# Kernel optimization log

Measured on AMD Instinct MI355X. Metric: run time of the kernel, lower is better.

## Reference

```python
import jax, jax.numpy as jnp
import numpy as np

DIM = 2048
NUM_HEADS = 16
HEAD_DIM = DIM // NUM_HEADS
WINDOW_SIZE = 3072
SCALE = HEAD_DIM ** (-0.5)
NEG_INF = -1e9


def setup_inputs() -> dict:
    key = jax.random.key(0)
    ks = jax.random.split(key, 6)
    B, N = 2, 2048
    x = jax.random.normal(ks[0], (B, N, DIM), dtype=jnp.float32)
    w_init = 0.02
    Wq = jax.random.normal(ks[1], (DIM, DIM), dtype=jnp.float32) * w_init
    Wk = jax.random.normal(ks[2], (DIM, DIM), dtype=jnp.float32) * w_init
    Wv = jax.random.normal(ks[3], (DIM, DIM), dtype=jnp.float32) * w_init
    Wo = jax.random.normal(ks[4], (DIM, DIM), dtype=jnp.float32) * w_init
    zeros = jnp.zeros((DIM,), dtype=jnp.float32)
    return {"x": x, "Wq": Wq, "bq": zeros, "Wk": Wk, "bk": zeros,
            "Wv": Wv, "bv": zeros, "Wo": Wo, "bo": zeros}


def _window_mask(q_len: int, kv_len: int) -> jnp.ndarray:
    # Faithful to SlidingWindowAttention._window_mask with causal=True:
    # row i allows j in [max(0, kv_len - window_size + i), i]; mask=True means blocked.
    i = jnp.arange(q_len)[:, None]
    j = jnp.arange(kv_len)[None, :]
    start = jnp.maximum(0, kv_len - WINDOW_SIZE + i)
    allowed = (j >= start) & (j <= i)  # second term is the causal triu complement
    return ~allowed  # [q_len, kv_len] bool, True = masked


def reference(x, Wq, bq, Wk, bk, Wv, bv, Wo, bo):
    B, N, C = x.shape
    H, D = NUM_HEADS, HEAD_DIM
    # torch nn.Linear: y = x @ W.T + b
    q = (x @ Wq.T + bq).reshape(B, N, H, D).transpose(0, 2, 1, 3)  # [B,H,N,D]
    k = (x @ Wk.T + bk).reshape(B, N, H, D).transpose(0, 2, 1, 3)
    v = (x @ Wv.T + bv).reshape(B, N, H, D).transpose(0, 2, 1, 3)

    scores = jnp.einsum('bhqd,bhkd->bhqk', q, k) * SCALE  # [B,H,N,N]
    mask = _window_mask(N, N)  # [N,N]
    scores = jnp.where(mask[None, None], NEG_INF, scores)
    attn = jax.nn.softmax(scores, axis=-1)
    out = jnp.einsum('bhqk,bhkd->bhqd', attn, v)  # [B,H,N,D]
    out = out.transpose(0, 2, 1, 3).reshape(B, N, C)
    return out @ Wo.T + bo
```

## Files before the change

### kernel.cpp

```cpp
#include <hip/hip_runtime.h>
#include <cstdint>

#define DIMC 2048
#define NSEQ 2048
#define BATCH 2
#define NH 16
#define HD 128
#define MROWS 4096
#define NQKV 6144
#define QSCALE 0.08838834764831845f

typedef float f32x4 __attribute__((ext_vector_type(4)));
typedef __bf16 bf16x8 __attribute__((ext_vector_type(8)));
typedef __bf16 bf16x4 __attribute__((ext_vector_type(4)));

__device__ __forceinline__ f32x4 mfma16(bf16x8 a, bf16x8 b, f32x4 c) {
  return __builtin_amdgcn_mfma_f32_16x16x32_bf16(a, b, c, 0, 0, 0);
}

typedef __attribute__((address_space(1))) void gvoid;
typedef __attribute__((address_space(3))) void ldsvoid;

__device__ __forceinline__ void async16(void* lds, const void* g) {
  __builtin_amdgcn_global_load_lds((gvoid*)(uintptr_t)g, (ldsvoid*)(uintptr_t)lds, 16, 0, 0);
}

__global__ __launch_bounds__(256) void cast_bf16(const float* __restrict__ src,
                                                 __bf16* __restrict__ dst, int n) {
  int i = (blockIdx.x * 256 + threadIdx.x) * 4;
  const int stride = gridDim.x * 1024;
  for (; i < n; i += stride) {
    const float4 v = *(const float4*)(src + i);
    bf16x4 o = {(__bf16)v.x, (__bf16)v.y, (__bf16)v.z, (__bf16)v.w};
    *(bf16x4*)(dst + i) = o;
  }
}

template <int EPI>
__global__ __launch_bounds__(256) void gemm_bt(
    const __bf16* __restrict__ A, const __bf16* __restrict__ Bm,
    __bf16* __restrict__ Qb, __bf16* __restrict__ Kb, __bf16* __restrict__ Vtb,
    const float* __restrict__ bias0, const float* __restrict__ bias1,
    const float* __restrict__ bias2, float* __restrict__ outp) {
  __shared__ __bf16 Al[128 * 32];
  __shared__ __bf16 Bl[128 * 32];
  const int tid = threadIdx.x;
  const int w = tid >> 6, l = tid & 63;
  const int a = l & 15, g = l >> 4;
  const int mbase = blockIdx.y * 128, nbase = blockIdx.x * 128;
  const int wr = w >> 1, wc = w & 1;

  f32x4 acc[4][4] = {};

  const char* Ag = (const char*)A +
      ((size_t)(mbase + w * 32 + (l >> 2)) * DIMC + (size_t)(l & 3) * 8) * 2;
  const char* Bg = (const char*)Bm +
      ((size_t)(nbase + w * 32 + (l >> 2)) * DIMC + (size_t)(l & 3) * 8) * 2;
  char* Alw = (char*)Al + w * 2048;
  char* Blw = (char*)Bl + w * 2048;

  for (int kt = 0; kt < DIMC / 32; ++kt) {
    const size_t ko = (size_t)kt * 64;
    async16(Alw, Ag + ko);
    async16(Alw + 1024, Ag + (size_t)16 * (DIMC * 2) + ko);
    async16(Blw, Bg + ko);
    async16(Blw + 1024, Bg + (size_t)16 * (DIMC * 2) + ko);
    __syncthreads();
    bf16x8 af[4], bf_[4];
#pragma unroll
    for (int m = 0; m < 4; ++m)
      af[m] = *(const bf16x8*)((const char*)Al + (wr * 64 + m * 16 + a) * 64 + g * 16);
#pragma unroll
    for (int n = 0; n < 4; ++n)
      bf_[n] = *(const bf16x8*)((const char*)Bl + (wc * 64 + n * 16 + a) * 64 + g * 16);
#pragma unroll
    for (int m = 0; m < 4; ++m)
#pragma unroll
      for (int n = 0; n < 4; ++n) acc[m][n] = mfma16(af[m], bf_[n], acc[m][n]);
    __syncthreads();
  }

  if constexpr (EPI == 0) {
    const int seg = nbase >> 11;
    const int cin = (nbase & 2047) + wc * 64;
    const float* bias = (seg == 0) ? bias0 : ((seg == 1) ? bias1 : bias2);
    const float scl = (seg == 0) ? QSCALE : 1.0f;
#pragma unroll
    for (int n = 0; n < 4; ++n) {
      const int c = cin + n * 16 + a;
      const float bb = bias[c];
      const int h = c >> 7, d = c & 127;
#pragma unroll
      for (int m = 0; m < 4; ++m) {
        const int mr = mbase + wr * 64 + m * 16 + g * 4;
        const int b_ = mr >> 11, sq = mr & 2047;
        f32x4 v = acc[m][n];
        if (seg == 2) {
          __bf16* dst = Vtb + ((size_t)(b_ * NH + h) * HD + d) * NSEQ + sq;
          bf16x4 pk = {(__bf16)(v[0] + bb), (__bf16)(v[1] + bb),
                       (__bf16)(v[2] + bb), (__bf16)(v[3] + bb)};
          *(bf16x4*)dst = pk;
        } else {
          __bf16* dst = ((seg == 0) ? Qb : Kb) +
                        ((size_t)(b_ * NH + h) * NSEQ + sq) * HD + d;
#pragma unroll
          for (int j = 0; j < 4; ++j) dst[(size_t)j * HD] = (__bf16)((v[j] + bb) * scl);
        }
      }
    }
  } else {
#pragma unroll
    for (int n = 0; n < 4; ++n) {
      const int c = nbase + wc * 64 + n * 16 + a;
      const float bb = bias0[c];
#pragma unroll
      for (int m = 0; m < 4; ++m) {
        const int mr = mbase + wr * 64 + m * 16 + g * 4;
        float* dst = outp + (size_t)mr * DIMC + c;
        f32x4 v = acc[m][n];
#pragma unroll
        for (int j = 0; j < 4; ++j) dst[(size_t)j * DIMC] = v[j] + bb;
      }
    }
  }
}

__global__ __launch_bounds__(256) void attn_swa(const __bf16* __restrict__ Qb,
                                                const __bf16* __restrict__ Kb,
                                                const __bf16* __restrict__ Vtb,
                                                __bf16* __restrict__ Ob) {
  __shared__ __bf16 Klds[64 * 128];
  __shared__ __bf16 Vlds[128 * 64];
  __shared__ __bf16 Plds[4 * 16 * 64];
  const int tid = threadIdx.x;
  const int w = tid >> 6, l = tid & 63;
  const int a = l & 15, g = l >> 4;
  const int bh = blockIdx.y;
  const int qbase = blockIdx.x * 64;
  const __bf16* Qg = Qb + (size_t)bh * NSEQ * HD + (size_t)qbase * HD;
  const __bf16* Kg = Kb + (size_t)bh * NSEQ * HD;
  const __bf16* Vg = Vtb + (size_t)bh * HD * NSEQ;

  bf16x8 qf[4];
#pragma unroll
  for (int s = 0; s < 4; ++s)
    qf[s] = *(const bf16x8*)(Qg + (size_t)(w * 16 + a) * HD + s * 32 + g * 8);

  float mrow[4] = {-1e38f, -1e38f, -1e38f, -1e38f};
  float lrow[4] = {0.f, 0.f, 0.f, 0.f};
  f32x4 o[8] = {};

  const int ktlo = (qbase >= 1024) ? ((qbase - 1024) >> 6) : 0;
  const int kthi = qbase >> 6;
  const int qmax = qbase + 63;

  for (int kt = ktlo; kt <= kthi; ++kt) {
    const int kb = kt * 64;
#pragma unroll
    for (int j = 0; j < 4; ++j) {
      const int off = j * 4096 + w * 1024 + l * 16;
      const int row = off >> 8;
      const int cg = ((off >> 4) & 15) ^ (row & 7);
      async16((char*)Klds + j * 4096 + w * 1024,
              (const char*)Kg + (size_t)(kb + row) * 256 + cg * 16);
    }
#pragma unroll
    for (int j = 0; j < 4; ++j) {
      const int off = j * 4096 + w * 1024 + l * 16;
      const int row = off >> 7;
      const int cg = ((off >> 4) & 7) ^ (row & 7);
      async16((char*)Vlds + j * 4096 + w * 1024,
              (const char*)Vg + (size_t)row * (NSEQ * 2) + (size_t)kb * 2 + cg * 16);
    }
    __syncthreads();

    const bool full = (kb >= qmax - 1024) && (kb + 63 <= qbase);
    f32x4 s4[4];
#pragma unroll
    for (int t = 0; t < 4; ++t) {
      f32x4 sc = {};
#pragma unroll
      for (int ds = 0; ds < 4; ++ds) {
        const int row = t * 16 + a;
        const int ch = (ds * 4 + g) ^ (row & 7);
        bf16x8 kf = *(const bf16x8*)((const char*)Klds + row * 256 + ch * 16);
        sc = mfma16(qf[ds], kf, sc);
      }
      s4[t] = sc;
    }
    if (!full) {
#pragma unroll
      for (int t = 0; t < 4; ++t)
#pragma unroll
        for (int i = 0; i < 4; ++i) {
          const int q = qbase + w * 16 + g * 4 + i;
          const int kv = kb + t * 16 + a;
          if (kv > q || kv + 1024 < q) s4[t][i] = -1e30f;
        }
    }
    float pm[4], corr[4], rs[4];
#pragma unroll
    for (int i = 0; i < 4; ++i)
      pm[i] = fmaxf(fmaxf(s4[0][i], s4[1][i]), fmaxf(s4[2][i], s4[3][i]));
#pragma unroll
    for (int i = 0; i < 4; ++i) {
      pm[i] = fmaxf(pm[i], __shfl_xor(pm[i], 1));
      pm[i] = fmaxf(pm[i], __shfl_xor(pm[i], 2));
      pm[i] = fmaxf(pm[i], __shfl_xor(pm[i], 4));
      pm[i] = fmaxf(pm[i], __shfl_xor(pm[i], 8));
      const float nm = fmaxf(mrow[i], pm[i]);
      corr[i] = __expf(mrow[i] - nm);
      mrow[i] = nm;
      rs[i] = 0.f;
    }
#pragma unroll
    for (int t = 0; t < 4; ++t)
#pragma unroll
      for (int i = 0; i < 4; ++i) {
        const float p = __expf(s4[t][i] - mrow[i]);
        s4[t][i] = p;
        rs[i] += p;
      }
#pragma unroll
    for (int i = 0; i < 4; ++i) {
      rs[i] += __shfl_xor(rs[i], 1);
      rs[i] += __shfl_xor(rs[i], 2);
      rs[i] += __shfl_xor(rs[i], 4);
      rs[i] += __shfl_xor(rs[i], 8);
      lrow[i] = lrow[i] * corr[i] + rs[i];
    }
#pragma unroll
    for (int n = 0; n < 8; ++n)
#pragma unroll
      for (int i = 0; i < 4; ++i) o[n][i] *= corr[i];
    char* Pw = (char*)Plds + w * 2048;
#pragma unroll
    for (int t = 0; t < 4; ++t)
#pragma unroll
      for (int i = 0; i < 4; ++i) {
        const int q = g * 4 + i;
        const int byte = (q * 128 + (t * 16 + a) * 2) ^ ((q & 7) << 4);
        *(__bf16*)(Pw + byte) = (__bf16)s4[t][i];
      }
#pragma unroll
    for (int ks = 0; ks < 2; ++ks) {
      const int ch = (ks * 4 + g) ^ (a & 7);
      bf16x8 pa = *(const bf16x8*)(Pw + a * 128 + ch * 16);
#pragma unroll
      for (int n = 0; n < 8; ++n) {
        const int row = n * 16 + a;
        const int vch = (ks * 4 + g) ^ (row & 7);
        bf16x8 vf = *(const bf16x8*)((const char*)Vlds + row * 128 + vch * 16);
        o[n] = mfma16(pa, vf, o[n]);
      }
    }
    __syncthreads();
  }

  const int b_ = bh >> 4, h = bh & 15;
  __bf16* Og = Ob + (size_t)(b_ * NSEQ + qbase + w * 16 + g * 4) * DIMC + h * HD;
#pragma unroll
  for (int i = 0; i < 4; ++i) {
    const float inv = 1.f / lrow[i];
#pragma unroll
    for (int n = 0; n < 8; ++n)
      Og[(size_t)i * DIMC + n * 16 + a] = (__bf16)(o[n][i] * inv);
  }
}

extern "C" void kernel_launch(void* const* d_in, const int* in_sizes, int n_in,
                              void* d_out, int out_size, void* d_ws, size_t ws_size,
                              hipStream_t stream) {
  const float* x = (const float*)d_in[0];
  const float* Wq = (const float*)d_in[1];
  const float* bq = (const float*)d_in[2];
  const float* Wk = (const float*)d_in[3];
  const float* bk = (const float*)d_in[4];
  const float* Wv = (const float*)d_in[5];
  const float* bv = (const float*)d_in[6];
  const float* Wo = (const float*)d_in[7];
  const float* bo = (const float*)d_in[8];
  float* out = (float*)d_out;

  char* ws = (char*)d_ws;
  __bf16* xb    = (__bf16*)(ws + 0);
  __bf16* Wqkvb = (__bf16*)(ws + 16777216);
  __bf16* Wob   = (__bf16*)(ws + 41943040);
  __bf16* Qb    = (__bf16*)(ws + 50331648);
  __bf16* Kb    = (__bf16*)(ws + 67108864);
  __bf16* Vtb   = (__bf16*)(ws + 83886080);
  __bf16* Ob    = xb;

  cast_bf16<<<dim3(2048), 256, 0, stream>>>(x, xb, MROWS * DIMC);
  cast_bf16<<<dim3(1024), 256, 0, stream>>>(Wq, Wqkvb, DIMC * DIMC);
  cast_bf16<<<dim3(1024), 256, 0, stream>>>(Wk, Wqkvb + (size_t)DIMC * DIMC, DIMC * DIMC);
  cast_bf16<<<dim3(1024), 256, 0, stream>>>(Wv, Wqkvb + (size_t)2 * DIMC * DIMC, DIMC * DIMC);
  cast_bf16<<<dim3(1024), 256, 0, stream>>>(Wo, Wob, DIMC * DIMC);

  gemm_bt<0><<<dim3(NQKV / 128, MROWS / 128), 256, 0, stream>>>(
      xb, Wqkvb, Qb, Kb, Vtb, bq, bk, bv, nullptr);

  attn_swa<<<dim3(NSEQ / 64, BATCH * NH), 256, 0, stream>>>(Qb, Kb, Vtb, Ob);

  gemm_bt<1><<<dim3(DIMC / 128, MROWS / 128), 256, 0, stream>>>(
      Ob, Wob, nullptr, nullptr, nullptr, bo, nullptr, nullptr, out);
}
```

Measured before the change: 291.2 us.

## Replace QKV GEMM with 256x256 double-buffered, swizzled, prioritized MFMA kernel

Adds a dedicated QKV projection kernel that uses 256x256 tiles, 512 threads, 128 KB of dynamic LDS with two buffers of 64-wide K slices, XOR-swizzled LDS layout, and fine-grained vmcnt/barrier interleaving of async global-to-LDS loads with MFMA phases under s_setprio. The goal is to hide global load latency and raise MFMA utilization relative to the old 128x128 single-buffered loop that synchronized twice per 32-wide K step. The output projection keeps the old kernel. The new kernel adds many barriers, high register pressure from 32 accumulators, and a grid of only 24x16 blocks.

Measured after the change: 319.4 us. 1.1x slower.

```diff
diff --git a/kernel.cpp b/kernel.cpp
--- a/kernel.cpp
+++ b/kernel.cpp
@@ -25,6 +25,9 @@
   __builtin_amdgcn_global_load_lds((gvoid*)(uintptr_t)g, (ldsvoid*)(uintptr_t)lds, 16, 0, 0);
 }
 
+#define BAR() asm volatile("s_barrier" ::: "memory")
+#define VMCNT(n) asm volatile("s_waitcnt vmcnt(" #n ")" ::: "memory")
+
 __global__ __launch_bounds__(256) void cast_bf16(const float* __restrict__ src,
                                                  __bf16* __restrict__ dst, int n) {
   int i = (blockIdx.x * 256 + threadIdx.x) * 4;
@@ -36,12 +39,135 @@
   }
 }
 
-template <int EPI>
-__global__ __launch_bounds__(256) void gemm_bt(
+#define RA 0
+#define RB 32768
+#define BUF1 65536
+
+#define READ_B(Bb) do { \
+    bfr[0][0]=ldf(Bb,rB,0);      bfr[0][1]=ldf(Bb,rB,1); \
+    bfr[1][0]=ldf(Bb,rB+16,0);   bfr[1][1]=ldf(Bb,rB+16,1); \
+    bfr[2][0]=ldf(Bb,rB+32,0);   bfr[2][1]=ldf(Bb,rB+32,1); \
+    bfr[3][0]=ldf(Bb,rB+48,0);   bfr[3][1]=ldf(Bb,rB+48,1); } while(0)
+
+#define READ_A(Ab,P) do { \
+    afr[0][0]=ldf(Ab,(P*2+0)*16+a,0); afr[0][1]=ldf(Ab,(P*2+0)*16+a,1); \
+    afr[1][0]=ldf(Ab,(P*2+1)*16+a,0); afr[1][1]=ldf(Ab,(P*2+1)*16+a,1); } while(0)
+
+#define DO_MFMA(P) do { __builtin_amdgcn_s_setprio(1); \
+    _Pragma("unroll") for (int f_=0; f_<2; ++f_) \
+    _Pragma("unroll") for (int n_=0; n_<4; ++n_) \
+    _Pragma("unroll") for (int k_=0; k_<2; ++k_) \
+      acc[P*2+f_][n_] = mfma16(afr[f_][k_], bfr[n_][k_], acc[P*2+f_][n_]); \
+    __builtin_amdgcn_s_setprio(0); } while(0)
+
+__global__ __launch_bounds__(512, 2) void qkv256(
     const __bf16* __restrict__ A, const __bf16* __restrict__ Bm,
     __bf16* __restrict__ Qb, __bf16* __restrict__ Kb, __bf16* __restrict__ Vtb,
-    const float* __restrict__ bias0, const float* __restrict__ bias1,
-    const float* __restrict__ bias2, float* __restrict__ outp) {
+    const float* __restrict__ bq, const float* __restrict__ bk,
+    const float* __restrict__ bv) {
+  extern __shared__ __align__(16) char Lds[];
+  const int tid = threadIdx.x;
+  const int l = tid & 63, w = tid >> 6;
+  const int a = l & 15, g = l >> 4;
+  const int wm = w >> 2, wn = w & 3;
+  const int mbase = blockIdx.y * 256, nbase = blockIdx.x * 256;
+  const int wbyte = w * 1024;
+  const char* Ag = (const char*)A;
+  const char* Bg = (const char*)Bm;
+  const int rB = (wn & 1) * 64 + a;
+
+  f32x4 acc[8][4] = {};
+  bf16x8 bfr[4][2], afr[2][2];
+
+  auto issue = [&](int bufofs, int regofs, const char* gmat, int grow0, int kt, int j) {
+    const int grow = grow0 + (j >> 1) * 128 + (j & 1) * 64 + (tid >> 3);
+    const int scol = ((tid & 7) * 16) ^ (((tid >> 5) & 1) << 5);
+    async16(Lds + bufofs + regofs + j * 8192 + wbyte,
+            gmat + (size_t)grow * (DIMC * 2) + kt * 128 + scol);
+  };
+  auto ldf = [&](const char* halfbase, int row, int ks) -> bf16x8 {
+    const int c = (ks * 64 + g * 16) ^ (((row >> 2) & 1) << 5);
+    return *(const bf16x8*)(halfbase + row * 128 + c);
+  };
+
+  issue(0, RB, Bg, nbase, 0, 0); issue(0, RB, Bg, nbase, 0, 1);
+  issue(0, RB, Bg, nbase, 0, 2); issue(0, RB, Bg, nbase, 0, 3);
+  issue(0, RA, Ag, mbase, 0, 0); issue(0, RA, Ag, mbase, 0, 2);
+  issue(0, RA, Ag, mbase, 0, 1); issue(0, RA, Ag, mbase, 0, 3);
+  issue(BUF1, RB, Bg, nbase, 1, 0); issue(BUF1, RB, Bg, nbase, 1, 1);
+  issue(BUF1, RB, Bg, nbase, 1, 2); issue(BUF1, RB, Bg, nbase, 1, 3);
+  issue(BUF1, RA, Ag, mbase, 1, 0); issue(BUF1, RA, Ag, mbase, 1, 2);
+
+  const char* A0 = Lds + wm * 16384;
+  const char* B0 = Lds + RB + (wn >> 1) * 16384;
+  const char* A1 = A0 + BUF1;
+  const char* B1 = B0 + BUF1;
+
+  for (int i = 0; i < 16; ++i) {
+    const bool more = (i < 15);
+    const int t2 = 2 * i + 2, t3 = 2 * i + 3;
+    issue(BUF1, RA, Ag, mbase, 2 * i + 1, 1);
+    issue(BUF1, RA, Ag, mbase, 2 * i + 1, 3);
+    VMCNT(8); BAR();
+    READ_B(B0); READ_A(A0, 0);
+    DO_MFMA(0); BAR();
+    READ_A(A0, 1);
+    if (more) { issue(0, RB, Bg, nbase, t2, 0); issue(0, RB, Bg, nbase, t2, 1); }
+    BAR(); DO_MFMA(1); BAR();
+    READ_A(A0, 2);
+    if (more) { issue(0, RB, Bg, nbase, t2, 2); issue(0, RB, Bg, nbase, t2, 3);
+                issue(0, RA, Ag, mbase, t2, 0); issue(0, RA, Ag, mbase, t2, 2); }
+    BAR(); DO_MFMA(2); BAR();
+    READ_A(A0, 3);
+    BAR(); DO_MFMA(3); BAR();
+    if (more) { issue(0, RA, Ag, mbase, t2, 1); issue(0, RA, Ag, mbase, t2, 3);
+                VMCNT(8); } else { VMCNT(0); }
+    BAR();
+    READ_B(B1); READ_A(A1, 0);
+    DO_MFMA(0); BAR();
+    READ_A(A1, 1);
+    if (more) { issue(BUF1, RB, Bg, nbase, t3, 0); issue(BUF1, RB, Bg, nbase, t3, 1); }
+    BAR(); DO_MFMA(1); BAR();
+    READ_A(A1, 2);
+    if (more) { issue(BUF1, RB, Bg, nbase, t3, 2); issue(BUF1, RB, Bg, nbase, t3, 3);
+                issue(BUF1, RA, Ag, mbase, t3, 0); issue(BUF1, RA, Ag, mbase, t3, 2); }
+    BAR(); DO_MFMA(2); BAR();
+    READ_A(A1, 3);
+    BAR(); DO_MFMA(3); BAR();
+  }
+
+  const int seg = nbase >> 11;
+  const int cin = (nbase & 2047) + wn * 64;
+  const float* bias = (seg == 0) ? bq : ((seg == 1) ? bk : bv);
+  const float scl = (seg == 0) ? QSCALE : 1.0f;
+#pragma unroll
+  for (int n = 0; n < 4; ++n) {
+    const int c = cin + n * 16 + a;
+    const float bb = bias[c];
+    const int h = c >> 7, d = c & 127;
+#pragma unroll
+    for (int m = 0; m < 8; ++m) {
+      const int mr = mbase + wm * 128 + m * 16 + g * 4;
+      const int b_ = mr >> 11, sq = mr & 2047;
+      f32x4 v = acc[m][n];
+      if (seg == 2) {
+        __bf16* dst = Vtb + ((size_t)(b_ * NH + h) * HD + d) * NSEQ + sq;
+        bf16x4 pk = {(__bf16)(v[0] + bb), (__bf16)(v[1] + bb),
+                     (__bf16)(v[2] + bb), (__bf16)(v[3] + bb)};
+        *(bf16x4*)dst = pk;
+      } else {
+        __bf16* dst = ((seg == 0) ? Qb : Kb) +
+                      ((size_t)(b_ * NH + h) * NSEQ + sq) * HD + d;
+#pragma unroll
+        for (int j = 0; j < 4; ++j) dst[(size_t)j * HD] = (__bf16)((v[j] + bb) * scl);
+      }
+    }
+  }
+}
+
+__global__ __launch_bounds__(256) void gemm_out(
+    const __bf16* __restrict__ A, const __bf16* __restrict__ Bm,
+    const float* __restrict__ bias0, float* __restrict__ outp) {
   __shared__ __bf16 Al[128 * 32];
   __shared__ __bf16 Bl[128 * 32];
   const int tid = threadIdx.x;
@@ -80,47 +206,17 @@
     __syncthreads();
   }
 
-  if constexpr (EPI == 0) {
-    const int seg = nbase >> 11;
-    const int cin = (nbase & 2047) + wc * 64;
-    const float* bias = (seg == 0) ? bias0 : ((seg == 1) ? bias1 : bias2);
-    const float scl = (seg == 0) ? QSCALE : 1.0f;
-#pragma unroll
-    for (int n = 0; n < 4; ++n) {
-      const int c = cin + n * 16 + a;
-      const float bb = bias[c];
-      const int h = c >> 7, d = c & 127;
-#pragma unroll
-      for (int m = 0; m < 4; ++m) {
-        const int mr = mbase + wr * 64 + m * 16 + g * 4;
-        const int b_ = mr >> 11, sq = mr & 2047;
-        f32x4 v = acc[m][n];
-        if (seg == 2) {
-          __bf16* dst = Vtb + ((size_t)(b_ * NH + h) * HD + d) * NSEQ + sq;
-          bf16x4 pk = {(__bf16)(v[0] + bb), (__bf16)(v[1] + bb),
-                       (__bf16)(v[2] + bb), (__bf16)(v[3] + bb)};
-          *(bf16x4*)dst = pk;
-        } else {
-          __bf16* dst = ((seg == 0) ? Qb : Kb) +
-                        ((size_t)(b_ * NH + h) * NSEQ + sq) * HD + d;
-#pragma unroll
-          for (int j = 0; j < 4; ++j) dst[(size_t)j * HD] = (__bf16)((v[j] + bb) * scl);
-        }
-      }
-    }
-  } else {
-#pragma unroll
-    for (int n = 0; n < 4; ++n) {
-      const int c = nbase + wc * 64 + n * 16 + a;
-      const float bb = bias0[c];
-#pragma unroll
-      for (int m = 0; m < 4; ++m) {
-        const int mr = mbase + wr * 64 + m * 16 + g * 4;
-        float* dst = outp + (size_t)mr * DIMC + c;
-        f32x4 v = acc[m][n];
-#pragma unroll
-        for (int j = 0; j < 4; ++j) dst[(size_t)j * DIMC] = v[j] + bb;
-      }
+#pragma unroll
+  for (int n = 0; n < 4; ++n) {
+    const int c = nbase + wc * 64 + n * 16 + a;
+    const float bb = bias0[c];
+#pragma unroll
+    for (int m = 0; m < 4; ++m) {
+      const int mr = mbase + wr * 64 + m * 16 + g * 4;
+      float* dst = outp + (size_t)mr * DIMC + c;
+      f32x4 v = acc[m][n];
+#pragma unroll
+      for (int j = 0; j < 4; ++j) dst[(size_t)j * DIMC] = v[j] + bb;
     }
   }
 }
@@ -291,17 +387,20 @@
   __bf16* Vtb   = (__bf16*)(ws + 83886080);
   __bf16* Ob    = xb;
 
+  (void)hipFuncSetAttribute((const void*)qkv256,
+                            hipFuncAttributeMaxDynamicSharedMemorySize, 131072);
+
   cast_bf16<<<dim3(2048), 256, 0, stream>>>(x, xb, MROWS * DIMC);
   cast_bf16<<<dim3(1024), 256, 0, stream>>>(Wq, Wqkvb, DIMC * DIMC);
   cast_bf16<<<dim3(1024), 256, 0, stream>>>(Wk, Wqkvb + (size_t)DIMC * DIMC, DIMC * DIMC);
   cast_bf16<<<dim3(1024), 256, 0, stream>>>(Wv, Wqkvb + (size_t)2 * DIMC * DIMC, DIMC * DIMC);
   cast_bf16<<<dim3(1024), 256, 0, stream>>>(Wo, Wob, DIMC * DIMC);
 
-  gemm_bt<0><<<dim3(NQKV / 128, MROWS / 128), 256, 0, stream>>>(
-      xb, Wqkvb, Qb, Kb, Vtb, bq, bk, bv, nullptr);
+  qkv256<<<dim3(NQKV / 256, MROWS / 256), 512, 131072, stream>>>(
+      xb, Wqkvb, Qb, Kb, Vtb, bq, bk, bv);
 
   attn_swa<<<dim3(NSEQ / 64, BATCH * NH), 256, 0, stream>>>(Qb, Kb, Vtb, Ob);
 
-  gemm_bt<1><<<dim3(DIMC / 128, MROWS / 128), 256, 0, stream>>>(
-      Ob, Wob, nullptr, nullptr, nullptr, bo, nullptr, nullptr, out);
-}
+  gemm_out<<<dim3(DIMC / 128, MROWS / 128), 256, 0, stream>>>(
+      Ob, Wob, bo, out);
+}
```

## Restructure sliding-window attention into larger double-buffered blocks; merge weight casts

Applied to the files above, without the earlier changes.

The attention kernel now handles 256 queries per block with 8 waves, each wave owning 32 query rows. K/V tiles are double-buffered in dynamic LDS so the next tile's async load overlaps compute, and each K/V tile is reused across four times as many queries. The four weight cast launches are merged into one 2D-grid launch. Tradeoffs: the grid is only 256 blocks using 96KB of LDS each, more registers per thread, and boundary tiles spanning a wider query range need masking.

Measured after the change: 293.4 us. Within noise of the previous version (+0.8%).

```diff
diff --git a/kernel.cpp b/kernel.cpp
--- a/kernel.cpp
+++ b/kernel.cpp
@@ -25,15 +25,30 @@
   __builtin_amdgcn_global_load_lds((gvoid*)(uintptr_t)g, (ldsvoid*)(uintptr_t)lds, 16, 0, 0);
 }
 
-__global__ __launch_bounds__(256) void cast_bf16(const float* __restrict__ src,
-                                                 __bf16* __restrict__ dst, int n) {
-  int i = (blockIdx.x * 256 + threadIdx.x) * 4;
-  const int stride = gridDim.x * 1024;
-  for (; i < n; i += stride) {
-    const float4 v = *(const float4*)(src + i);
-    bf16x4 o = {(__bf16)v.x, (__bf16)v.y, (__bf16)v.z, (__bf16)v.w};
-    *(bf16x4*)(dst + i) = o;
-  }
+#define BAR() asm volatile("s_barrier" ::: "memory")
+#define VMCNT0() asm volatile("s_waitcnt vmcnt(0)" ::: "memory")
+
+__global__ __launch_bounds__(256) void cast_x(const float* __restrict__ src,
+                                              __bf16* __restrict__ dst) {
+  const int i = (blockIdx.x * 256 + threadIdx.x) * 4;
+  const float4 v = *(const float4*)(src + i);
+  bf16x4 o = {(__bf16)v.x, (__bf16)v.y, (__bf16)v.z, (__bf16)v.w};
+  *(bf16x4*)(dst + i) = o;
+}
+
+__global__ __launch_bounds__(256) void cast_w(const float* __restrict__ Wq,
+                                              const float* __restrict__ Wk,
+                                              const float* __restrict__ Wv,
+                                              const float* __restrict__ Wo,
+                                              __bf16* __restrict__ Wqkvb,
+                                              __bf16* __restrict__ Wob) {
+  const int m = blockIdx.y;
+  const float* s = (m == 0) ? Wq : (m == 1) ? Wk : (m == 2) ? Wv : Wo;
+  __bf16* d = (m == 3) ? Wob : Wqkvb + (size_t)m * DIMC * DIMC;
+  const int i = (blockIdx.x * 256 + threadIdx.x) * 4;
+  const float4 v = *(const float4*)(s + i);
+  bf16x4 o = {(__bf16)v.x, (__bf16)v.y, (__bf16)v.z, (__bf16)v.w};
+  *(bf16x4*)(d + i) = o;
 }
 
 template <int EPI>
@@ -125,146 +140,174 @@
   }
 }
 
-__global__ __launch_bounds__(256) void attn_swa(const __bf16* __restrict__ Qb,
-                                                const __bf16* __restrict__ Kb,
-                                                const __bf16* __restrict__ Vtb,
-                                                __bf16* __restrict__ Ob) {
-  __shared__ __bf16 Klds[64 * 128];
-  __shared__ __bf16 Vlds[128 * 64];
-  __shared__ __bf16 Plds[4 * 16 * 64];
+__global__ __launch_bounds__(512) void attn_swa2(const __bf16* __restrict__ Qb,
+                                                 const __bf16* __restrict__ Kb,
+                                                 const __bf16* __restrict__ Vtb,
+                                                 __bf16* __restrict__ Ob) {
+  extern __shared__ __align__(16) char AL[];
   const int tid = threadIdx.x;
   const int w = tid >> 6, l = tid & 63;
   const int a = l & 15, g = l >> 4;
   const int bh = blockIdx.y;
-  const int qbase = blockIdx.x * 64;
-  const __bf16* Qg = Qb + (size_t)bh * NSEQ * HD + (size_t)qbase * HD;
-  const __bf16* Kg = Kb + (size_t)bh * NSEQ * HD;
-  const __bf16* Vg = Vtb + (size_t)bh * HD * NSEQ;
-
-  bf16x8 qf[4];
-#pragma unroll
-  for (int s = 0; s < 4; ++s)
-    qf[s] = *(const bf16x8*)(Qg + (size_t)(w * 16 + a) * HD + s * 32 + g * 8);
-
-  float mrow[4] = {-1e38f, -1e38f, -1e38f, -1e38f};
-  float lrow[4] = {0.f, 0.f, 0.f, 0.f};
-  f32x4 o[8] = {};
+  const int qbase = blockIdx.x * 256;
+  const __bf16* Qg = Qb + (size_t)bh * NSEQ * HD;
+  const char* Kg = (const char*)(Kb + (size_t)bh * NSEQ * HD);
+  const char* Vg = (const char*)(Vtb + (size_t)bh * HD * NSEQ);
+
+  bf16x8 qf[2][4];
+#pragma unroll
+  for (int qi = 0; qi < 2; ++qi)
+#pragma unroll
+    for (int s = 0; s < 4; ++s)
+      qf[qi][s] = *(const bf16x8*)(Qg + (size_t)(qbase + w * 32 + qi * 16 + a) * HD + s * 32 + g * 8);
+
+  float mrow[2][4], lrow[2][4];
+#pragma unroll
+  for (int qi = 0; qi < 2; ++qi)
+#pragma unroll
+    for (int i = 0; i < 4; ++i) { mrow[qi][i] = -1e38f; lrow[qi][i] = 0.f; }
+  f32x4 o[2][8] = {};
 
   const int ktlo = (qbase >= 1024) ? ((qbase - 1024) >> 6) : 0;
-  const int kthi = qbase >> 6;
-  const int qmax = qbase + 63;
+  const int kthi = (qbase + 255) >> 6;
+
+  auto stage = [&](int b, int kt) {
+    const int kb2 = kt * 64;
+    char* Kl = AL + b * 32768;
+    char* Vl = AL + b * 32768 + 16384;
+#pragma unroll
+    for (int j = 0; j < 2; ++j) {
+      const int row = j * 32 + (tid >> 4);
+      const int ch = (tid & 15) ^ ((tid >> 4) & 7);
+      async16(Kl + j * 8192 + w * 1024, Kg + (size_t)(kb2 + row) * 256 + ch * 16);
+    }
+#pragma unroll
+    for (int j = 0; j < 2; ++j) {
+      const int row = j * 64 + (tid >> 3);
+      const int ch = (tid & 7) ^ ((tid >> 3) & 7);
+      async16(Vl + j * 8192 + w * 1024,
+              Vg + (size_t)row * (NSEQ * 2) + (size_t)kb2 * 2 + ch * 16);
+    }
+  };
+
+  stage(0, ktlo);
+  VMCNT0(); BAR();
+  int buf = 0;
+  char* Pw = AL + 65536 + w * 4096;
 
   for (int kt = ktlo; kt <= kthi; ++kt) {
-    const int kb = kt * 64;
-#pragma unroll
-    for (int j = 0; j < 4; ++j) {
-      const int off = j * 4096 + w * 1024 + l * 16;
-      const int row = off >> 8;
-      const int cg = ((off >> 4) & 15) ^ (row & 7);
-      async16((char*)Klds + j * 4096 + w * 1024,
-              (const char*)Kg + (size_t)(kb + row) * 256 + cg * 16);
-    }
-#pragma unroll
-    for (int j = 0; j < 4; ++j) {
-      const int off = j * 4096 + w * 1024 + l * 16;
-      const int row = off >> 7;
-      const int cg = ((off >> 4) & 7) ^ (row & 7);
-      async16((char*)Vlds + j * 4096 + w * 1024,
-              (const char*)Vg + (size_t)row * (NSEQ * 2) + (size_t)kb * 2 + cg * 16);
-    }
-    __syncthreads();
-
-    const bool full = (kb >= qmax - 1024) && (kb + 63 <= qbase);
-    f32x4 s4[4];
-#pragma unroll
-    for (int t = 0; t < 4; ++t) {
-      f32x4 sc = {};
-#pragma unroll
-      for (int ds = 0; ds < 4; ++ds) {
-        const int row = t * 16 + a;
-        const int ch = (ds * 4 + g) ^ (row & 7);
-        bf16x8 kf = *(const bf16x8*)((const char*)Klds + row * 256 + ch * 16);
-        sc = mfma16(qf[ds], kf, sc);
-      }
-      s4[t] = sc;
-    }
+    if (kt < kthi) stage(buf ^ 1, kt + 1);
+    const char* Kl = AL + buf * 32768;
+    const char* Vl = AL + buf * 32768 + 16384;
+    const int kb2 = kt * 64;
+    const bool full = (kb2 >= qbase + 255 - 1024) && (kb2 + 63 <= qbase);
+
+    f32x4 s4[2][4];
+#pragma unroll
+    for (int qi = 0; qi < 2; ++qi)
+#pragma unroll
+      for (int t = 0; t < 4; ++t) {
+        f32x4 sc = {};
+#pragma unroll
+        for (int ds = 0; ds < 4; ++ds) {
+          const int row = t * 16 + a;
+          const int ch = (ds * 4 + g) ^ (row & 7);
+          bf16x8 kf = *(const bf16x8*)(Kl + row * 256 + ch * 16);
+          sc = mfma16(qf[qi][ds], kf, sc);
+        }
+        s4[qi][t] = sc;
+      }
+
     if (!full) {
 #pragma unroll
+      for (int qi = 0; qi < 2; ++qi)
+#pragma unroll
+        for (int t = 0; t < 4; ++t)
+#pragma unroll
+          for (int i = 0; i < 4; ++i) {
+            const int q = qbase + w * 32 + qi * 16 + g * 4 + i;
+            const int kv = kb2 + t * 16 + a;
+            if (kv > q || kv + 1024 < q) s4[qi][t][i] = -1e30f;
+          }
+    }
+
+#pragma unroll
+    for (int qi = 0; qi < 2; ++qi) {
+      float pm[4], corr[4], rs[4];
+#pragma unroll
+      for (int i = 0; i < 4; ++i)
+        pm[i] = fmaxf(fmaxf(s4[qi][0][i], s4[qi][1][i]),
+                      fmaxf(s4[qi][2][i], s4[qi][3][i]));
+#pragma unroll
+      for (int i = 0; i < 4; ++i) {
+        pm[i] = fmaxf(pm[i], __shfl_xor(pm[i], 1));
+        pm[i] = fmaxf(pm[i], __shfl_xor(pm[i], 2));
+        pm[i] = fmaxf(pm[i], __shfl_xor(pm[i], 4));
+        pm[i] = fmaxf(pm[i], __shfl_xor(pm[i], 8));
+        const float nm = fmaxf(mrow[qi][i], pm[i]);
+        corr[i] = __expf(mrow[qi][i] - nm);
+        mrow[qi][i] = nm;
+        rs[i] = 0.f;
+      }
+#pragma unroll
       for (int t = 0; t < 4; ++t)
 #pragma unroll
         for (int i = 0; i < 4; ++i) {
-          const int q = qbase + w * 16 + g * 4 + i;
-          const int kv = kb + t * 16 + a;
-          if (kv > q || kv + 1024 < q) s4[t][i] = -1e30f;
-        }
-    }
-    float pm[4], corr[4], rs[4];
-#pragma unroll
-    for (int i = 0; i < 4; ++i)
-      pm[i] = fmaxf(fmaxf(s4[0][i], s4[1][i]), fmaxf(s4[2][i], s4[3][i]));
+          const float p = __expf(s4[qi][t][i] - mrow[qi][i]);
+          s4[qi][t][i] = p;
+          rs[i] += p;
+        }
+#pragma unroll
+      for (int i = 0; i < 4; ++i) {
+        rs[i] += __shfl_xor(rs[i], 1);
+        rs[i] += __shfl_xor(rs[i], 2);
+        rs[i] += __shfl_xor(rs[i], 4);
+        rs[i] += __shfl_xor(rs[i], 8);
+        lrow[qi][i] = lrow[qi][i] * corr[i] + rs[i];
+      }
+#pragma unroll
+      for (int n = 0; n < 8; ++n)
+#pragma unroll
+        for (int i = 0; i < 4; ++i) o[qi][n][i] *= corr[i];
+#pragma unroll
+      for (int t = 0; t < 4; ++t)
+#pragma unroll
+        for (int i = 0; i < 4; ++i) {
+          const int q8 = qi * 16 + g * 4 + i;
+          const int byte = (q8 * 128 + (t * 16 + a) * 2) ^ ((q8 & 7) << 4);
+          *(__bf16*)(Pw + byte) = (__bf16)s4[qi][t][i];
+        }
+    }
+#pragma unroll
+    for (int qi = 0; qi < 2; ++qi)
+#pragma unroll
+      for (int ks = 0; ks < 2; ++ks) {
+        const int pb = ((qi * 16 + a) * 128 + ks * 64 + g * 16) ^ ((a & 7) << 4);
+        bf16x8 pa = *(const bf16x8*)(Pw + pb);
+#pragma unroll
+        for (int n = 0; n < 8; ++n) {
+          const int row = n * 16 + a;
+          const int vch = (ks * 4 + g) ^ (a & 7);
+          bf16x8 vf = *(const bf16x8*)(Vl + row * 128 + vch * 16);
+          o[qi][n] = mfma16(pa, vf, o[qi][n]);
+        }
+      }
+
+    VMCNT0(); BAR();
+    buf ^= 1;
+  }
+
+  const int b_ = bh >> 4, h = bh & 15;
+#pragma unroll
+  for (int qi = 0; qi < 2; ++qi) {
+    __bf16* Og = Ob + (size_t)(b_ * NSEQ + qbase + w * 32 + qi * 16 + g * 4) * DIMC + h * HD;
 #pragma unroll
     for (int i = 0; i < 4; ++i) {
-      pm[i] = fmaxf(pm[i], __shfl_xor(pm[i], 1));
-      pm[i] = fmaxf(pm[i], __shfl_xor(pm[i], 2));
-      pm[i] = fmaxf(pm[i], __shfl_xor(pm[i], 4));
-      pm[i] = fmaxf(pm[i], __shfl_xor(pm[i], 8));
-      const float nm = fmaxf(mrow[i], pm[i]);
-      corr[i] = __expf(mrow[i] - nm);
-      mrow[i] = nm;
-      rs[i] = 0.f;
-    }
-#pragma unroll
-    for (int t = 0; t < 4; ++t)
-#pragma unroll
-      for (int i = 0; i < 4; ++i) {
-        const float p = __expf(s4[t][i] - mrow[i]);
-        s4[t][i] = p;
-        rs[i] += p;
-      }
-#pragma unroll
-    for (int i = 0; i < 4; ++i) {
-      rs[i] += __shfl_xor(rs[i], 1);
-      rs[i] += __shfl_xor(rs[i], 2);
-      rs[i] += __shfl_xor(rs[i], 4);
-      rs[i] += __shfl_xor(rs[i], 8);
-      lrow[i] = lrow[i] * corr[i] + rs[i];
-    }
-#pragma unroll
-    for (int n = 0; n < 8; ++n)
-#pragma unroll
-      for (int i = 0; i < 4; ++i) o[n][i] *= corr[i];
-    char* Pw = (char*)Plds + w * 2048;
-#pragma unroll
-    for (int t = 0; t < 4; ++t)
-#pragma unroll
-      for (int i = 0; i < 4; ++i) {
-        const int q = g * 4 + i;
-        const int byte = (q * 128 + (t * 16 + a) * 2) ^ ((q & 7) << 4);
-        *(__bf16*)(Pw + byte) = (__bf16)s4[t][i];
-      }
-#pragma unroll
-    for (int ks = 0; ks < 2; ++ks) {
-      const int ch = (ks * 4 + g) ^ (a & 7);
-      bf16x8 pa = *(const bf16x8*)(Pw + a * 128 + ch * 16);
-#pragma unroll
-      for (int n = 0; n < 8; ++n) {
-        const int row = n * 16 + a;
-        const int vch = (ks * 4 + g) ^ (row & 7);
-        bf16x8 vf = *(const bf16x8*)((const char*)Vlds + row * 128 + vch * 16);
-        o[n] = mfma16(pa, vf, o[n]);
-      }
-    }
-    __syncthreads();
-  }
-
-  const int b_ = bh >> 4, h = bh & 15;
-  __bf16* Og = Ob + (size_t)(b_ * NSEQ + qbase + w * 16 + g * 4) * DIMC + h * HD;
-#pragma unroll
-  for (int i = 0; i < 4; ++i) {
-    const float inv = 1.f / lrow[i];
-#pragma unroll
-    for (int n = 0; n < 8; ++n)
-      Og[(size_t)i * DIMC + n * 16 + a] = (__bf16)(o[n][i] * inv);
+      const float inv = 1.f / lrow[qi][i];
+#pragma unroll
+      for (int n = 0; n < 8; ++n)
+        Og[(size_t)i * DIMC + n * 16 + a] = (__bf16)(o[qi][n][i] * inv);
+    }
   }
 }
 
@@ -291,16 +334,16 @@
   __bf16* Vtb   = (__bf16*)(ws + 83886080);
   __bf16* Ob    = xb;
 
-  cast_bf16<<<dim3(2048), 256, 0, stream>>>(x, xb, MROWS * DIMC);
-  cast_bf16<<<dim3(1024), 256, 0, stream>>>(Wq, Wqkvb, DIMC * DIMC);
-  cast_bf16<<<dim3(1024), 256, 0, stream>>>(Wk, Wqkvb + (size_t)DIMC * DIMC, DIMC * DIMC);
-  cast_bf16<<<dim3(1024), 256, 0, stream>>>(Wv, Wqkvb + (size_t)2 * DIMC * DIMC, DIMC * DIMC);
-  cast_bf16<<<dim3(1024), 256, 0, stream>>>(Wo, Wob, DIMC * DIMC);
+  (void)hipFuncSetAttribute((const void*)attn_swa2,
+                            hipFuncAttributeMaxDynamicSharedMemorySize, 98304);
+
+  cast_x<<<dim3(MROWS * DIMC / 1024), 256, 0, stream>>>(x, xb);
+  cast_w<<<dim3(DIMC * DIMC / 1024, 4), 256, 0, stream>>>(Wq, Wk, Wv, Wo, Wqkvb, Wob);
 
   gemm_bt<0><<<dim3(NQKV / 128, MROWS / 128), 256, 0, stream>>>(
       xb, Wqkvb, Qb, Kb, Vtb, bq, bk, bv, nullptr);
 
-  attn_swa<<<dim3(NSEQ / 64, BATCH * NH), 256, 0, stream>>>(Qb, Kb, Vtb, Ob);
+  attn_swa2<<<dim3(NSEQ / 256, BATCH * NH), 512, 98304, stream>>>(Qb, Kb, Vtb, Ob);
 
   gemm_bt<1><<<dim3(DIMC / 128, MROWS / 128), 256, 0, stream>>>(
       Ob, Wob, nullptr, nullptr, nullptr, bo, nullptr, nullptr, out);
```
